# Performance work log

Hardware: AMD Instinct MI355X
Metric: run time of the kernel (lower is better)

## Reference

```python
import jax, jax.numpy as jnp
import numpy as np

EMBED_DIM = 512
NUM_HEADS = 8
HEAD_DIM = EMBED_DIM // NUM_HEADS
K_NEIGH = 3
SEQ_N = 16384
BATCH = 4


def setup_inputs() -> dict:
    key = jax.random.key(0)
    ks = jax.random.split(key, 12)
    x = jax.random.normal(ks[0], (BATCH, SEQ_N, EMBED_DIM), dtype=jnp.float32)
    neighbor_table = jax.random.randint(ks[1], (K_NEIGH, SEQ_N), 0, SEQ_N, dtype=jnp.int64)
    s = 0.02
    Wq = jax.random.normal(ks[2], (EMBED_DIM, EMBED_DIM), jnp.float32) * s
    bq = jnp.zeros((EMBED_DIM,), jnp.float32)
    Wk = jax.random.normal(ks[3], (EMBED_DIM, EMBED_DIM), jnp.float32) * s
    bk = jnp.zeros((EMBED_DIM,), jnp.float32)
    Wv = jax.random.normal(ks[4], (EMBED_DIM, EMBED_DIM), jnp.float32) * s
    bv = jnp.zeros((EMBED_DIM,), jnp.float32)
    Wo = jax.random.normal(ks[5], (EMBED_DIM, EMBED_DIM), jnp.float32) * s
    bo = jnp.zeros((EMBED_DIM,), jnp.float32)
    return {"x": x, "neighbor_table": neighbor_table,
            "Wq": Wq, "bq": bq, "Wk": Wk, "bk": bk,
            "Wv": Wv, "bv": bv, "Wo": Wo, "bo": bo}


def reference(x, neighbor_table, Wq, bq, Wk, bk, Wv, bv, Wo, bo):
    B, N, C = x.shape
    H, d = NUM_HEADS, HEAD_DIM
    scale = d ** (-0.5)
    # buffers derived from neighbor_table (matches module __init__)
    valid = (neighbor_table != -1)                      # (K, N)
    idx = jnp.clip(neighbor_table, 0)                   # (K, N)

    # projections; nn.Linear: y = x @ W.T + b
    def proj(W, b):
        return (jnp.einsum('bnc,oc->bno', x, W) + b).reshape(B, N, H, d).transpose(0, 2, 1, 3)  # (B,H,N,d)

    q = proj(Wq, bq)
    k = proj(Wk, bk)
    v = proj(Wv, bv)

    # gather neighbors: (B, H, K, N, d)
    k_nb = k[:, :, idx, :]
    v_nb = v[:, :, idx, :]

    # scores over head_dim: (B, H, K, N)
    scores = jnp.einsum('bhnd,bhknd->bhkn', q, k_nb) * scale
    scores = jnp.where(valid[None, None], scores, -jnp.inf)
    attn = jax.nn.softmax(scores, axis=2)               # softmax over K neighbors
    # dropout is identity (eval / p used only at train)

    out = jnp.einsum('bhkn,bhknd->bhnd', attn, v_nb)    # (B,H,N,d)
    out = out.transpose(0, 2, 1, 3).reshape(B, N, C)
    out = jnp.einsum('bnc,oc->bno', out, Wo) + bo
    return out
```

## Files before the change

kernel.cpp:

```cpp
#include <hip/hip_runtime.h>
#include <stdint.h>

#define SEQN 16384
#define NBATCH 4

typedef __attribute__((ext_vector_type(8))) __bf16 bf16x8;
typedef __attribute__((ext_vector_type(4))) float f32x4;
typedef __attribute__((ext_vector_type(4))) unsigned int u32x4;

__device__ __forceinline__ unsigned int f2bf(float f) {
  unsigned int x = __builtin_bit_cast(unsigned int, f);
  x = x + 0x7fffu + ((x >> 16) & 1u);
  return x >> 16;
}
__device__ __forceinline__ float bf2f(unsigned int lo) {
  return __builtin_bit_cast(float, lo << 16);
}

__device__ __forceinline__ void gload_lds16(const unsigned short* g, unsigned char* l) {
  __builtin_amdgcn_global_load_lds(
      (const __attribute__((address_space(1))) unsigned int*)g,
      (__attribute__((address_space(3))) unsigned int*)l, 16, 0, 0);
}

template<bool OUT_BF16>
__global__ __launch_bounds__(256, 4)
void gemm_bt(const unsigned short* __restrict__ A,
             const unsigned short* __restrict__ Bt,
             const float* __restrict__ bias,
             void* __restrict__ Cout,
             int Ncols, int K)
{
  __shared__ __align__(16) unsigned char lA[128 * 64 * 2];
  __shared__ __align__(16) unsigned char lB[128 * 64 * 2];
  const int tid = threadIdx.x;
  const int lane = tid & 63;
  const int wid = tid >> 6;
  const int wr = (wid >> 1) * 64;
  const int wc = (wid & 1) * 64;
  const int nbx = Ncols >> 7;
  const int bid = (int)blockIdx.x;
  const int cpx = (int)gridDim.x >> 3;
  const int swz = (bid & 7) * cpx + (bid >> 3);
  const int bx = swz % nbx;
  const int by = swz / nbx;
  const long row0 = (long)by << 7;
  const int col0 = bx << 7;

  f32x4 acc[4][4];
#pragma unroll
  for (int i = 0; i < 4; ++i)
#pragma unroll
    for (int j = 0; j < 4; ++j) acc[i][j] = (f32x4)0.0f;

  for (int kt = 0; kt < K; kt += 64) {
#pragma unroll
    for (int i = 0; i < 4; ++i) {
      const int f = i * 256 + tid;
      const int r = f >> 3;
      const int cd = (f & 7) ^ (r & 7);
      gload_lds16(A + (row0 + r) * (long)K + kt + cd * 8, lA + f * 16);
      gload_lds16(Bt + (long)(col0 + r) * K + kt + cd * 8, lB + f * 16);
    }
    __syncthreads();
#pragma unroll
    for (int kk = 0; kk < 2; ++kk) {
      bf16x8 af[4], bfv[4];
#pragma unroll
      for (int fm = 0; fm < 4; ++fm) {
        const int row = wr + fm * 16 + (lane & 15);
        const int ch = (kk * 4 + (lane >> 4)) ^ (row & 7);
        af[fm] = __builtin_bit_cast(bf16x8, *(const u32x4*)(lA + row * 128 + ch * 16));
      }
#pragma unroll
      for (int fn = 0; fn < 4; ++fn) {
        const int row = wc + fn * 16 + (lane & 15);
        const int ch = (kk * 4 + (lane >> 4)) ^ (row & 7);
        bfv[fn] = __builtin_bit_cast(bf16x8, *(const u32x4*)(lB + row * 128 + ch * 16));
      }
#pragma unroll
      for (int fm = 0; fm < 4; ++fm)
#pragma unroll
        for (int fn = 0; fn < 4; ++fn)
          acc[fm][fn] = __builtin_amdgcn_mfma_f32_16x16x32_bf16(af[fm], bfv[fn], acc[fm][fn], 0, 0, 0);
    }
    __syncthreads();
  }

#pragma unroll
  for (int fn = 0; fn < 4; ++fn) {
    const int n = col0 + wc + fn * 16 + (lane & 15);
    const float bn = bias[n];
#pragma unroll
    for (int fm = 0; fm < 4; ++fm) {
      const long mbase = row0 + wr + fm * 16 + ((lane >> 4) << 2);
#pragma unroll
      for (int j = 0; j < 4; ++j) {
        const float v = acc[fm][fn][j] + bn;
        if constexpr (OUT_BF16)
          ((unsigned short*)Cout)[(mbase + j) * (long)Ncols + n] = (unsigned short)f2bf(v);
        else
          ((float*)Cout)[(mbase + j) * (long)Ncols + n] = v;
      }
    }
  }
}

__global__ __launch_bounds__(256)
void nbr_attn(const unsigned short* __restrict__ qkv,
              const int* __restrict__ nbr,
              unsigned short* __restrict__ aout)
{
  const int wid = (int)((blockIdx.x * 256 + threadIdx.x) >> 6);
  const int lane = threadIdx.x & 63;
  const int n = wid & (SEQN - 1);
  const int b = wid >> 14;

  const unsigned short* qrow = qkv + (size_t)wid * 1536;
  const u32x4 qraw = *(const u32x4*)(qrow + lane * 8);

  int t0 = nbr[n];
  int t1 = nbr[SEQN + n];
  int t2 = nbr[2 * SEQN + n];
  bool val[3] = {t0 != -1, t1 != -1, t2 != -1};
  const unsigned short* base = qkv + (size_t)b * SEQN * 1536 + 512 + lane * 8;
  const unsigned short* k0 = base + (size_t)(t0 > 0 ? t0 : 0) * 1536;
  const unsigned short* k1 = base + (size_t)(t1 > 0 ? t1 : 0) * 1536;
  const unsigned short* k2 = base + (size_t)(t2 > 0 ? t2 : 0) * 1536;
  u32x4 kraw[3], vraw[3];
  kraw[0] = *(const u32x4*)k0;
  vraw[0] = *(const u32x4*)(k0 + 512);
  kraw[1] = *(const u32x4*)k1;
  vraw[1] = *(const u32x4*)(k1 + 512);
  kraw[2] = *(const u32x4*)k2;
  vraw[2] = *(const u32x4*)(k2 + 512);

  float qv[8];
#pragma unroll
  for (int i = 0; i < 4; ++i) {
    qv[2 * i] = bf2f(qraw[i] & 0xffffu);
    qv[2 * i + 1] = bf2f(qraw[i] >> 16);
  }
  float s[3];
#pragma unroll
  for (int k = 0; k < 3; ++k) {
    float d = 0.f;
#pragma unroll
    for (int i = 0; i < 4; ++i)
      d += qv[2 * i] * bf2f(kraw[k][i] & 0xffffu) + qv[2 * i + 1] * bf2f(kraw[k][i] >> 16);
    d += __shfl_xor(d, 1);
    d += __shfl_xor(d, 2);
    d += __shfl_xor(d, 4);
    s[k] = d * 0.125f;
  }
  float m = -3.0e38f;
#pragma unroll
  for (int k = 0; k < 3; ++k)
    if (val[k]) m = fmaxf(m, s[k]);
  float e[3], sum = 0.f;
#pragma unroll
  for (int k = 0; k < 3; ++k) {
    e[k] = val[k] ? __expf(s[k] - m) : 0.f;
    sum += e[k];
  }
  const float inv = sum > 0.f ? 1.f / sum : 0.f;
  float acc[8] = {0.f, 0.f, 0.f, 0.f, 0.f, 0.f, 0.f, 0.f};
#pragma unroll
  for (int k = 0; k < 3; ++k) {
    const float w = e[k] * inv;
#pragma unroll
    for (int i = 0; i < 4; ++i) {
      acc[2 * i] += w * bf2f(vraw[k][i] & 0xffffu);
      acc[2 * i + 1] += w * bf2f(vraw[k][i] >> 16);
    }
  }
  u32x4 o;
#pragma unroll
  for (int i = 0; i < 4; ++i)
    o[i] = f2bf(acc[2 * i]) | (f2bf(acc[2 * i + 1]) << 16);
  *(u32x4*)(aout + (size_t)wid * 512 + lane * 8) = o;
}

__global__ __launch_bounds__(256)
void cvt_f32_bf16(const float* __restrict__ in, unsigned short* __restrict__ out, int n8) {
  int i = blockIdx.x * 256 + threadIdx.x;
  const int stride = gridDim.x * 256;
  for (; i < n8; i += stride) {
    const float4* p = (const float4*)(in + (size_t)i * 8);
    const float4 a = p[0], c = p[1];
    u32x4 o;
    o[0] = f2bf(a.x) | (f2bf(a.y) << 16);
    o[1] = f2bf(a.z) | (f2bf(a.w) << 16);
    o[2] = f2bf(c.x) | (f2bf(c.y) << 16);
    o[3] = f2bf(c.z) | (f2bf(c.w) << 16);
    *(u32x4*)(out + (size_t)i * 8) = o;
  }
}

__global__ __launch_bounds__(256)
void prep_w(const float* __restrict__ Wq, const float* __restrict__ Wk,
            const float* __restrict__ Wv, const float* __restrict__ Wo,
            const float* __restrict__ bq, const float* __restrict__ bk,
            const float* __restrict__ bv,
            unsigned short* __restrict__ wf, unsigned short* __restrict__ wo,
            float* __restrict__ biasf)
{
  const int i = blockIdx.x * 256 + threadIdx.x;
  const int stride = gridDim.x * 256;
  for (int t = i; t < 262144; t += stride) {
    wf[t] = (unsigned short)f2bf(Wq[t]);
    wf[262144 + t] = (unsigned short)f2bf(Wk[t]);
    wf[524288 + t] = (unsigned short)f2bf(Wv[t]);
    wo[t] = (unsigned short)f2bf(Wo[t]);
  }
  if (i < 512) {
    biasf[i] = bq[i];
    biasf[512 + i] = bk[i];
    biasf[1024 + i] = bv[i];
  }
}

extern "C" void kernel_launch(void* const* d_in, const int* in_sizes, int n_in,
                              void* d_out, int out_size, void* d_ws, size_t ws_size,
                              hipStream_t stream) {
  const float* x  = (const float*)d_in[0];
  const int* nbr  = (const int*)d_in[1];
  const float* Wq = (const float*)d_in[2];
  const float* bq = (const float*)d_in[3];
  const float* Wk = (const float*)d_in[4];
  const float* bk = (const float*)d_in[5];
  const float* Wv = (const float*)d_in[6];
  const float* bv = (const float*)d_in[7];
  const float* Wo = (const float*)d_in[8];
  const float* bo = (const float*)d_in[9];
  float* out = (float*)d_out;
  unsigned char* ws = (unsigned char*)d_ws;

  unsigned short* xb  = (unsigned short*)(ws);
  unsigned short* qkv = (unsigned short*)(ws + 67108864UL);
  unsigned short* wf  = (unsigned short*)(ws + 268435456UL);
  unsigned short* wo  = (unsigned short*)(ws + 270008320UL);
  float* biasf        = (float*)(ws + 270532608UL);

  cvt_f32_bf16<<<4096, 256, 0, stream>>>(x, xb, 33554432 / 8);
  prep_w<<<1024, 256, 0, stream>>>(Wq, Wk, Wv, Wo, bq, bk, bv, wf, wo, biasf);
  gemm_bt<true><<<dim3(512 * 12), 256, 0, stream>>>(xb, wf, biasf, qkv, 1536, 512);
  nbr_attn<<<16384, 256, 0, stream>>>(qkv, nbr, xb);
  gemm_bt<false><<<dim3(512 * 4), 256, 0, stream>>>(xb, wo, bo, out, 512, 512);
}
```

Measured before the change: 284.3 us.

## Add 4-stage LDS ring-buffered GEMM for QKV projection

Introduces gemm_ring, a QKV projection GEMM that splits K into 32-wide slices and keeps a 4-deep ring of LDS buffers, issuing global-to-LDS loads three stages ahead and using explicit vmcnt waits, raw barriers and sched_barrier/setprio around the MFMA block. This is meant to overlap global memory latency with MFMA compute, where the old kernel waited on each 64-wide tile before computing. It uses 64KB of LDS and launch bounds of 2 blocks per CU, so occupancy drops. K is hardcoded to 512.

New measurement: 300.7 us. 5.8% more time.

```diff
diff --git a/kernel.cpp b/kernel.cpp
--- a/kernel.cpp
+++ b/kernel.cpp
@@ -21,6 +21,141 @@
   __builtin_amdgcn_global_load_lds(
       (const __attribute__((address_space(1))) unsigned int*)g,
       (__attribute__((address_space(3))) unsigned int*)l, 16, 0, 0);
+}
+
+__device__ __forceinline__ void barrier_raw() {
+  asm volatile("" ::: "memory");
+  __builtin_amdgcn_s_barrier();
+  asm volatile("" ::: "memory");
+}
+
+template<bool OUT_BF16>
+__global__ __launch_bounds__(256, 2)
+void gemm_ring(const unsigned short* __restrict__ A,
+               const unsigned short* __restrict__ Bt,
+               const float* __restrict__ bias,
+               void* __restrict__ Cout,
+               int Ncols)
+{
+  __shared__ __align__(16) unsigned char smem[65536];
+  const int K = 512;
+  const int tid = threadIdx.x;
+  const int lane = tid & 63;
+  const int wid = tid >> 6;
+  const int wr = (wid >> 1) * 64;
+  const int wc = (wid & 1) * 64;
+  const int nbx = Ncols >> 7;
+  const int bid = (int)blockIdx.x;
+  const int cpx = (int)gridDim.x >> 3;
+  const int swz = (bid & 7) * cpx + (bid >> 3);
+  const int bx = swz % nbx;
+  const int by = swz / nbx;
+  const long row0 = (long)by << 7;
+  const int col0 = bx << 7;
+
+  int srcA0, srcA1, srcB0, srcB1;
+  {
+    const int r0 = tid >> 2, c0 = (tid & 3) ^ ((r0 >> 1) & 3);
+    const int r1 = 64 + (tid >> 2), c1 = (tid & 3) ^ ((r1 >> 1) & 3);
+    srcA0 = (int)(row0 + r0) * K + c0 * 8;
+    srcA1 = (int)(row0 + r1) * K + c1 * 8;
+    srcB0 = (col0 + r0) * K + c0 * 8;
+    srcB1 = (col0 + r1) * K + c1 * 8;
+  }
+
+  int aoff[4], boff[4];
+#pragma unroll
+  for (int fm = 0; fm < 4; ++fm) {
+    const int r = wr + fm * 16 + (lane & 15);
+    aoff[fm] = r * 64 + ((((lane >> 4)) ^ ((r >> 1) & 3)) << 4);
+  }
+#pragma unroll
+  for (int fn = 0; fn < 4; ++fn) {
+    const int r = wc + fn * 16 + (lane & 15);
+    boff[fn] = r * 64 + ((((lane >> 4)) ^ ((r >> 1) & 3)) << 4);
+  }
+
+  f32x4 acc[4][4];
+#pragma unroll
+  for (int i = 0; i < 4; ++i)
+#pragma unroll
+    for (int j = 0; j < 4; ++j) acc[i][j] = (f32x4)0.0f;
+
+#define STAGE(t)                                                            \
+  {                                                                         \
+    unsigned char* buf_ = smem + ((t) & 3) * 16384;                         \
+    const int kt_ = (t) * 32;                                               \
+    gload_lds16(A + srcA0 + kt_, buf_ + tid * 16);                          \
+    gload_lds16(A + srcA1 + kt_, buf_ + 4096 + tid * 16);                   \
+    gload_lds16(Bt + srcB0 + kt_, buf_ + 8192 + tid * 16);                  \
+    gload_lds16(Bt + srcB1 + kt_, buf_ + 12288 + tid * 16);                 \
+  }
+
+#define DSREAD(t)                                                           \
+  const unsigned char* buf_ = smem + ((t) & 3) * 16384;                     \
+  bf16x8 af[4], bfv[4];                                                     \
+  _Pragma("unroll")                                                         \
+  for (int fm = 0; fm < 4; ++fm)                                            \
+    af[fm] = __builtin_bit_cast(bf16x8, *(const u32x4*)(buf_ + aoff[fm]));  \
+  _Pragma("unroll")                                                         \
+  for (int fn = 0; fn < 4; ++fn)                                            \
+    bfv[fn] = __builtin_bit_cast(bf16x8,                                    \
+                  *(const u32x4*)(buf_ + 8192 + boff[fn]));
+
+#define MFMA16()                                                            \
+  asm volatile("s_waitcnt lgkmcnt(0)" ::: "memory");                        \
+  __builtin_amdgcn_sched_barrier(0);                                        \
+  __builtin_amdgcn_s_setprio(1);                                            \
+  _Pragma("unroll")                                                         \
+  for (int fm = 0; fm < 4; ++fm)                                            \
+    _Pragma("unroll")                                                       \
+    for (int fn = 0; fn < 4; ++fn)                                          \
+      acc[fm][fn] = __builtin_amdgcn_mfma_f32_16x16x32_bf16(                \
+          af[fm], bfv[fn], acc[fm][fn], 0, 0, 0);                           \
+  __builtin_amdgcn_s_setprio(0);                                            \
+  __builtin_amdgcn_sched_barrier(0);
+
+#define WAITVM(n)                                                           \
+  __builtin_amdgcn_sched_barrier(0);                                        \
+  asm volatile("s_waitcnt vmcnt(" #n ")" ::: "memory");                     \
+  __builtin_amdgcn_sched_barrier(0);
+
+  STAGE(0); STAGE(1); STAGE(2);
+  WAITVM(8);
+  barrier_raw();
+  for (int t = 0; t < 13; ++t) {
+    WAITVM(4);
+    STAGE(t + 3);
+    DSREAD(t);
+    barrier_raw();
+    MFMA16();
+    barrier_raw();
+  }
+  { WAITVM(4); DSREAD(13); barrier_raw(); MFMA16(); barrier_raw(); }
+  { WAITVM(0); DSREAD(14); barrier_raw(); MFMA16(); barrier_raw(); }
+  { DSREAD(15); MFMA16(); }
+#undef STAGE
+#undef DSREAD
+#undef MFMA16
+#undef WAITVM
+
+#pragma unroll
+  for (int fn = 0; fn < 4; ++fn) {
+    const int n = col0 + wc + fn * 16 + (lane & 15);
+    const float bn = bias[n];
+#pragma unroll
+    for (int fm = 0; fm < 4; ++fm) {
+      const long mbase = row0 + wr + fm * 16 + ((lane >> 4) << 2);
+#pragma unroll
+      for (int j = 0; j < 4; ++j) {
+        const float v = acc[fm][fn][j] + bn;
+        if constexpr (OUT_BF16)
+          ((unsigned short*)Cout)[(mbase + j) * (long)Ncols + n] = (unsigned short)f2bf(v);
+        else
+          ((float*)Cout)[(mbase + j) * (long)Ncols + n] = v;
+      }
+    }
+  }
 }
 
 template<bool OUT_BF16>
@@ -244,7 +379,7 @@
 
   cvt_f32_bf16<<<4096, 256, 0, stream>>>(x, xb, 33554432 / 8);
   prep_w<<<1024, 256, 0, stream>>>(Wq, Wk, Wv, Wo, bq, bk, bv, wf, wo, biasf);
-  gemm_bt<true><<<dim3(512 * 12), 256, 0, stream>>>(xb, wf, biasf, qkv, 1536, 512);
+  gemm_ring<true><<<dim3(512 * 12), 256, 0, stream>>>(xb, wf, biasf, qkv, 1536);
   nbr_attn<<<16384, 256, 0, stream>>>(qkv, nbr, xb);
   gemm_bt<false><<<dim3(512 * 4), 256, 0, stream>>>(xb, wo, bo, out, 512, 512);
 }
```
